# Kernel tuning notes

Hardware: AMD Instinct MI355X
Metric: run time of the kernel (lower is better)

## Reference

```python
import jax, jax.numpy as jnp
import numpy as np

BITS = 8
EPS = 1e-08


def _scalar_quantize_maxabs(x, scale, bits, eps):
    # clamp(round(x / scale), -qmax, qmax) with a fixed (precomputed) scalar scale
    qmax = float(2 ** (bits - 1) - 1)
    s = jnp.maximum(scale, eps)
    return jnp.clip(jnp.round(x / s), -qmax, qmax)


def setup_inputs() -> dict:
    key = jax.random.key(0)
    k1, k2, k3 = jax.random.split(key, 3)
    B, S, D_in, D_out = 4, 2048, 2048, 2048
    hidden_states = jax.random.normal(k1, (B, S, D_in), dtype=jnp.float32)
    # weight_quantized holds low-bit integer values stored as float (as produced by the quantizer)
    qmax = float(2 ** (BITS - 1) - 1)
    weight_quantized = jnp.round(
        jnp.clip(jax.random.normal(k2, (D_in, D_out), dtype=jnp.float32) * (qmax / 3.0), -qmax, qmax)
    )
    x_scale = jnp.asarray(0.05, dtype=jnp.float32)
    bias = jax.random.normal(k3, (D_out,), dtype=jnp.float32)
    return {
        "hidden_states": hidden_states,
        "weight_quantized": weight_quantized,
        "x_scale": x_scale,
        "bias": bias,
    }


def reference(hidden_states, weight_quantized, x_scale, bias) -> jnp.ndarray:
    original_shape = hidden_states.shape[:-1]
    input_dim = hidden_states.shape[-1]
    x_flat = hidden_states.reshape(-1, input_dim)  # [B*S, D_in]
    x_q = _scalar_quantize_maxabs(x_flat, x_scale.reshape(()), BITS, EPS)
    out = x_q.astype(weight_quantized.dtype) @ weight_quantized  # [B*S, D_out]
    out = out + bias.astype(out.dtype)[None, :]
    return out.astype(hidden_states.dtype).reshape(*original_shape, weight_quantized.shape[1])
```

## Files before the change

kernel.cpp:

```cpp
#include <hip/hip_runtime.h>
#include <cstdint>
#include <cstddef>

#define MDIM 8192
#define NDIM 2048
#define KDIM 2048

constexpr int BM = 128, BN = 128, BK = 128;

typedef int v4i __attribute__((ext_vector_type(4)));

__device__ __forceinline__ void async_ld16(const void* g, void* l) {
    __builtin_amdgcn_global_load_lds(
        (const __attribute__((address_space(1))) int*)g,
        (__attribute__((address_space(3))) int*)l,
        16, 0, 0);
}

__device__ __forceinline__ uint32_t q8(float x, float inv) {
    float q = fminf(fmaxf(rintf(x * inv), -127.f), 127.f);
    return (uint32_t)((int)q) & 0xffu;
}

__global__ void quant_x_kernel(const float4* __restrict__ x, uint4* __restrict__ xq,
                               const float* __restrict__ scale_p) {
    int t = blockIdx.x * blockDim.x + threadIdx.x;
    float inv = 1.0f / fmaxf(scale_p[0], 1e-8f);
    uint32_t w[4];
#pragma unroll
    for (int j = 0; j < 4; ++j) {
        float4 v = x[t * 4 + j];
        w[j] = q8(v.x, inv) | (q8(v.y, inv) << 8) | (q8(v.z, inv) << 16) | (q8(v.w, inv) << 24);
    }
    xq[t] = make_uint4(w[0], w[1], w[2], w[3]);
}

__global__ void quant_wt_kernel(const float* __restrict__ w, int8_t* __restrict__ wt) {
    __shared__ int8_t t[64][65];
    const int k0 = blockIdx.y * 64;
    const int n0 = blockIdx.x * 64;
    const int tid = threadIdx.x;
    const int rr = tid >> 4;
    const int c4 = (tid & 15) * 4;
    for (int p = 0; p < 4; ++p) {
        int r = rr + p * 16;
        float4 v = *(const float4*)&w[(size_t)(k0 + r) * NDIM + n0 + c4];
        t[c4 + 0][r] = (int8_t)rintf(v.x);
        t[c4 + 1][r] = (int8_t)rintf(v.y);
        t[c4 + 2][r] = (int8_t)rintf(v.z);
        t[c4 + 3][r] = (int8_t)rintf(v.w);
    }
    __syncthreads();
    for (int p = 0; p < 4; ++p) {
        int c = rr + p * 16;
        uint32_t o = (uint32_t)(uint8_t)t[c][c4 + 0]
                   | ((uint32_t)(uint8_t)t[c][c4 + 1] << 8)
                   | ((uint32_t)(uint8_t)t[c][c4 + 2] << 16)
                   | ((uint32_t)(uint8_t)t[c][c4 + 3] << 24);
        *(uint32_t*)&wt[(size_t)(n0 + c) * KDIM + k0 + c4] = o;
    }
}

__global__ __launch_bounds__(256, 4)
void gemm_i8_kernel(const int8_t* __restrict__ A,
                    const int8_t* __restrict__ Bt,
                    const float* __restrict__ bias,
                    float* __restrict__ C) {
    __shared__ alignas(16) int8_t lA[BM * BK];
    __shared__ alignas(16) int8_t lB[BN * BK];

    const int tid  = threadIdx.x;
    const int lane = tid & 63;
    const int wave = tid >> 6;
    const int wm   = wave & 1;
    const int wn   = wave >> 1;
    const int m0   = blockIdx.y * BM;
    const int n0   = blockIdx.x * BN;

    const int srow = lane >> 3;
    const int schk = (lane & 7) ^ srow;
    const int8_t* gA = A  + (size_t)(m0 + wave * 32 + srow) * KDIM + schk * 16;
    const int8_t* gB = Bt + (size_t)(n0 + wave * 32 + srow) * KDIM + schk * 16;
    int8_t* lAw = &lA[wave * 4096];
    int8_t* lBw = &lB[wave * 4096];

    const int quad = lane >> 4;
    const int lr   = lane & 15;
    const int sw   = lr & 7;
    const int arow = (wm * 64 + lr) * BK;
    const int brow = (wn * 64 + lr) * BK;

    v4i acc[4][4];
#pragma unroll
    for (int i = 0; i < 4; ++i)
#pragma unroll
        for (int j = 0; j < 4; ++j)
            acc[i][j] = (v4i){0, 0, 0, 0};

    for (int k0 = 0; k0 < KDIM; k0 += BK) {
        __syncthreads();
#pragma unroll
        for (int i = 0; i < 4; ++i) {
            async_ld16(gA + (size_t)i * 8 * KDIM, lAw + i * 1024);
            async_ld16(gB + (size_t)i * 8 * KDIM, lBw + i * 1024);
        }
        gA += BK; gB += BK;
        __syncthreads();

#pragma unroll
        for (int s = 0; s < 2; ++s) {
            const int cs = ((4 * s + quad) ^ sw) * 16;
            v4i af[4], bf[4];
#pragma unroll
            for (int i = 0; i < 4; ++i)
                af[i] = *(const v4i*)&lA[arow + i * 16 * BK + cs];
#pragma unroll
            for (int j = 0; j < 4; ++j)
                bf[j] = *(const v4i*)&lB[brow + j * 16 * BK + cs];
#pragma unroll
            for (int i = 0; i < 4; ++i)
#pragma unroll
                for (int j = 0; j < 4; ++j)
                    acc[i][j] = __builtin_amdgcn_mfma_i32_16x16x64_i8(af[i], bf[j], acc[i][j], 0, 0, 0);
        }
    }

    const int crow = m0 + wm * 64 + quad * 4;
    const int ccol = n0 + wn * 64 + lr;
    float bj[4];
#pragma unroll
    for (int j = 0; j < 4; ++j) bj[j] = bias[ccol + j * 16];
#pragma unroll
    for (int i = 0; i < 4; ++i)
#pragma unroll
        for (int j = 0; j < 4; ++j)
#pragma unroll
            for (int r = 0; r < 4; ++r)
                C[(size_t)(crow + i * 16 + r) * NDIM + (ccol + j * 16)] = (float)acc[i][j][r] + bj[j];
}

extern "C" void kernel_launch(void* const* d_in, const int* in_sizes, int n_in,
                              void* d_out, int out_size, void* d_ws, size_t ws_size,
                              hipStream_t stream) {
    const float* x    = (const float*)d_in[0];
    const float* w    = (const float*)d_in[1];
    const float* xs   = (const float*)d_in[2];
    const float* bias = (const float*)d_in[3];
    float* out = (float*)d_out;

    int8_t* xq = (int8_t*)d_ws;
    int8_t* wt = xq + (size_t)MDIM * KDIM;

    quant_x_kernel<<<((size_t)MDIM * KDIM / 16) / 256, 256, 0, stream>>>(
        (const float4*)x, (uint4*)xq, xs);
    quant_wt_kernel<<<dim3(NDIM / 64, KDIM / 64), 256, 0, stream>>>(w, wt);
    gemm_i8_kernel<<<dim3(NDIM / BN, MDIM / BM), 256, 0, stream>>>(xq, wt, bias, out);
}
```

Baseline: 168.7 us.

## Double-buffer LDS in int8 GEMM with BK=64 and simplify quantize kernels

The GEMM main loop now uses two LDS buffers at BK=64, so the async global-to-LDS load of the next K tile is issued before the MFMAs on the current tile and needs one barrier per iteration instead of two. The swizzle pattern is adapted to the 64-byte rows. The x quantize kernel now has each thread handle one float4 instead of four, and the weight transpose kernel packs bytes into 32-bit words in shared memory. The aim is to hide global load latency behind compute, at the cost of a doubled LDS footprint and twice as many K iterations.

New measurement: 168.1 us. About the same (-0.3%).

```diff
diff --git a/kernel.cpp b/kernel.cpp
--- a/kernel.cpp
+++ b/kernel.cpp
@@ -6,7 +6,7 @@
 #define NDIM 2048
 #define KDIM 2048
 
-constexpr int BM = 128, BN = 128, BK = 128;
+constexpr int BM = 128, BN = 128, BK = 64;
 
 typedef int v4i __attribute__((ext_vector_type(4)));
 
@@ -22,42 +22,42 @@
     return (uint32_t)((int)q) & 0xffu;
 }
 
-__global__ void quant_x_kernel(const float4* __restrict__ x, uint4* __restrict__ xq,
+__global__ void quant_x_kernel(const float4* __restrict__ x, uint32_t* __restrict__ xq,
                                const float* __restrict__ scale_p) {
-    int t = blockIdx.x * blockDim.x + threadIdx.x;
+    int i = blockIdx.x * blockDim.x + threadIdx.x;
     float inv = 1.0f / fmaxf(scale_p[0], 1e-8f);
-    uint32_t w[4];
-#pragma unroll
-    for (int j = 0; j < 4; ++j) {
-        float4 v = x[t * 4 + j];
-        w[j] = q8(v.x, inv) | (q8(v.y, inv) << 8) | (q8(v.z, inv) << 16) | (q8(v.w, inv) << 24);
-    }
-    xq[t] = make_uint4(w[0], w[1], w[2], w[3]);
+    float4 v = x[i];
+    xq[i] = q8(v.x, inv) | (q8(v.y, inv) << 8) | (q8(v.z, inv) << 16) | (q8(v.w, inv) << 24);
 }
 
-__global__ void quant_wt_kernel(const float* __restrict__ w, int8_t* __restrict__ wt) {
-    __shared__ int8_t t[64][65];
+__global__ void quant_wt_kernel(const float* __restrict__ w, uint32_t* __restrict__ wt) {
+    __shared__ uint32_t t[64][17];
     const int k0 = blockIdx.y * 64;
     const int n0 = blockIdx.x * 64;
     const int tid = threadIdx.x;
-    const int rr = tid >> 4;
-    const int c4 = (tid & 15) * 4;
+    const int rr  = tid >> 4;
+    const int c4  = (tid & 15) * 4;
+#pragma unroll
     for (int p = 0; p < 4; ++p) {
         int r = rr + p * 16;
         float4 v = *(const float4*)&w[(size_t)(k0 + r) * NDIM + n0 + c4];
-        t[c4 + 0][r] = (int8_t)rintf(v.x);
-        t[c4 + 1][r] = (int8_t)rintf(v.y);
-        t[c4 + 2][r] = (int8_t)rintf(v.z);
-        t[c4 + 3][r] = (int8_t)rintf(v.w);
+        uint32_t pk = (uint32_t)((int)rintf(v.x) & 0xff)
+                    | ((uint32_t)((int)rintf(v.y) & 0xff) << 8)
+                    | ((uint32_t)((int)rintf(v.z) & 0xff) << 16)
+                    | ((uint32_t)((int)rintf(v.w) & 0xff) << 24);
+        t[r][c4 >> 2] = pk;
     }
     __syncthreads();
+#pragma unroll
     for (int p = 0; p < 4; ++p) {
         int c = rr + p * 16;
-        uint32_t o = (uint32_t)(uint8_t)t[c][c4 + 0]
-                   | ((uint32_t)(uint8_t)t[c][c4 + 1] << 8)
-                   | ((uint32_t)(uint8_t)t[c][c4 + 2] << 16)
-                   | ((uint32_t)(uint8_t)t[c][c4 + 3] << 24);
-        *(uint32_t*)&wt[(size_t)(n0 + c) * KDIM + k0 + c4] = o;
+        uint32_t o = 0;
+#pragma unroll
+        for (int j = 0; j < 4; ++j) {
+            uint32_t b = (t[c4 + j][c >> 2] >> ((c & 3) * 8)) & 0xffu;
+            o |= b << (j * 8);
+        }
+        wt[((size_t)(n0 + c) * KDIM + k0 + c4) >> 2] = o;
     }
 }
 
@@ -66,8 +66,8 @@
                     const int8_t* __restrict__ Bt,
                     const float* __restrict__ bias,
                     float* __restrict__ C) {
-    __shared__ alignas(16) int8_t lA[BM * BK];
-    __shared__ alignas(16) int8_t lB[BN * BK];
+    __shared__ alignas(16) int8_t lA[2][BM * BK];
+    __shared__ alignas(16) int8_t lB[2][BN * BK];
 
     const int tid  = threadIdx.x;
     const int lane = tid & 63;
@@ -77,18 +77,17 @@
     const int m0   = blockIdx.y * BM;
     const int n0   = blockIdx.x * BN;
 
-    const int srow = lane >> 3;
-    const int schk = (lane & 7) ^ srow;
+    const int srow = lane >> 2;
+    const int schk = (lane & 3) ^ ((srow >> 1) & 3);
     const int8_t* gA = A  + (size_t)(m0 + wave * 32 + srow) * KDIM + schk * 16;
     const int8_t* gB = Bt + (size_t)(n0 + wave * 32 + srow) * KDIM + schk * 16;
-    int8_t* lAw = &lA[wave * 4096];
-    int8_t* lBw = &lB[wave * 4096];
+    const int lwo = wave * 2048;
 
     const int quad = lane >> 4;
     const int lr   = lane & 15;
-    const int sw   = lr & 7;
-    const int arow = (wm * 64 + lr) * BK;
-    const int brow = (wn * 64 + lr) * BK;
+    const int fchk = (quad ^ ((lr >> 1) & 3)) * 16;
+    const int aoff = (wm * 64 + lr) * BK + fchk;
+    const int boff = (wn * 64 + lr) * BK + fchk;
 
     v4i acc[4][4];
 #pragma unroll
@@ -97,33 +96,41 @@
         for (int j = 0; j < 4; ++j)
             acc[i][j] = (v4i){0, 0, 0, 0};
 
-    for (int k0 = 0; k0 < KDIM; k0 += BK) {
+#define STAGE(buf, kof)                                                        \
+    do {                                                                       \
+        async_ld16(gA + (kof), &lA[buf][lwo]);                                 \
+        async_ld16(gA + (kof) + (size_t)16 * KDIM, &lA[buf][lwo + 1024]);      \
+        async_ld16(gB + (kof), &lB[buf][lwo]);                                 \
+        async_ld16(gB + (kof) + (size_t)16 * KDIM, &lB[buf][lwo + 1024]);      \
+    } while (0)
+
+#define COMPUTE(buf)                                                           \
+    do {                                                                       \
+        v4i af[4], bf[4];                                                      \
+        _Pragma("unroll")                                                      \
+        for (int i = 0; i < 4; ++i)                                            \
+            af[i] = *(const v4i*)&lA[buf][aoff + i * 16 * BK];                 \
+        _Pragma("unroll")                                                      \
+        for (int j = 0; j < 4; ++j)                                            \
+            bf[j] = *(const v4i*)&lB[buf][boff + j * 16 * BK];                 \
+        _Pragma("unroll")                                                      \
+        for (int i = 0; i < 4; ++i)                                            \
+            _Pragma("unroll")                                                  \
+            for (int j = 0; j < 4; ++j)                                        \
+                acc[i][j] = __builtin_amdgcn_mfma_i32_16x16x64_i8(             \
+                    af[i], bf[j], acc[i][j], 0, 0, 0);                         \
+    } while (0)
+
+    STAGE(0, 0);
+    int kof = BK;
+    for (int it = 0; it < KDIM / BK - 1; ++it) {
         __syncthreads();
-#pragma unroll
-        for (int i = 0; i < 4; ++i) {
-            async_ld16(gA + (size_t)i * 8 * KDIM, lAw + i * 1024);
-            async_ld16(gB + (size_t)i * 8 * KDIM, lBw + i * 1024);
-        }
-        gA += BK; gB += BK;
-        __syncthreads();
-
-#pragma unroll
-        for (int s = 0; s < 2; ++s) {
-            const int cs = ((4 * s + quad) ^ sw) * 16;
-            v4i af[4], bf[4];
-#pragma unroll
-            for (int i = 0; i < 4; ++i)
-                af[i] = *(const v4i*)&lA[arow + i * 16 * BK + cs];
-#pragma unroll
-            for (int j = 0; j < 4; ++j)
-                bf[j] = *(const v4i*)&lB[brow + j * 16 * BK + cs];
-#pragma unroll
-            for (int i = 0; i < 4; ++i)
-#pragma unroll
-                for (int j = 0; j < 4; ++j)
-                    acc[i][j] = __builtin_amdgcn_mfma_i32_16x16x64_i8(af[i], bf[j], acc[i][j], 0, 0, 0);
-        }
+        STAGE((it + 1) & 1, kof);
+        kof += BK;
+        COMPUTE(it & 1);
     }
+    __syncthreads();
+    COMPUTE((KDIM / BK - 1) & 1);
 
     const int crow = m0 + wm * 64 + quad * 4;
     const int ccol = n0 + wn * 64 + lr;
@@ -151,8 +158,8 @@
     int8_t* xq = (int8_t*)d_ws;
     int8_t* wt = xq + (size_t)MDIM * KDIM;
 
-    quant_x_kernel<<<((size_t)MDIM * KDIM / 16) / 256, 256, 0, stream>>>(
-        (const float4*)x, (uint4*)xq, xs);
-    quant_wt_kernel<<<dim3(NDIM / 64, KDIM / 64), 256, 0, stream>>>(w, wt);
+    quant_x_kernel<<<((size_t)MDIM * KDIM / 4) / 256, 256, 0, stream>>>(
+        (const float4*)x, (uint32_t*)xq, xs);
+    quant_wt_kernel<<<dim3(NDIM / 64, KDIM / 64), 256, 0, stream>>>(w, (uint32_t*)wt);
     gemm_i8_kernel<<<dim3(NDIM / BN, MDIM / BM), 256, 0, stream>>>(xq, wt, bias, out);
 }
```
